# Kernel tuning notes

Measured on AMD Instinct MI355X. Metric: run time of the kernel, lower is better.

The kernel has to match this reference:

```python
import jax, jax.numpy as jnp
import numpy as np

VOCAB = 50257
D_MODEL = 1024
RANK = 64
V1, V2 = 225, 224   # ceil(sqrt(vocab)), ceil(vocab/v1)
D1, D2 = 32, 32     # ceil(sqrt(d_model)), ceil(d_model/d1)
B, L = 4, 4096


def setup_inputs() -> dict:
    key = jax.random.key(0)
    ks = jax.random.split(key, 4)
    input_ids = jax.random.randint(ks[0], (B, L), 0, VOCAB, dtype=jnp.int32)
    core1_q = jax.random.randint(ks[1], (V1, 1, RANK, D1), -128, 128, dtype=jnp.int32).astype(jnp.int8)
    core2_q = jax.random.randint(ks[2], (V2, RANK, 1, D2), -128, 128, dtype=jnp.int32).astype(jnp.int8)
    phase_shift = jax.random.normal(ks[3], (RANK,), dtype=jnp.float32) * 0.02
    return {
        "input_ids": input_ids,
        "core1_q": core1_q,
        "core1_scale": jnp.float32(0.01),
        "core1_zp": jnp.float32(0.0),
        "core2_q": core2_q,
        "core2_scale": jnp.float32(0.01),
        "core2_zp": jnp.float32(0.0),
        "phase_shift": phase_shift,
    }


def reference(input_ids, core1_q, core1_scale, core1_zp, core2_q, core2_scale, core2_zp, phase_shift):
    # token index -> (row in core1, row in core2)
    idx1 = jnp.clip(input_ids // V2, 0, V1 - 1)  # [B, L]
    idx2 = jnp.clip(input_ids % V2, 0, V2 - 1)   # [B, L]

    # gather int8 rows first, then dequantize: (q - zp) * scale (same math as
    # dequantizing full cores then gathering, but avoids touching unused rows)
    c1 = (core1_q[idx1, 0].astype(jnp.float32) - core1_zp) * core1_scale     # [B, L, R, D1]
    c2 = (core2_q[idx2, :, 0].astype(jnp.float32) - core2_zp) * core2_scale  # [B, L, R, D2]

    # phase modulation on core1 along the rank axis
    c1 = c1 * jnp.cos(phase_shift)[None, None, :, None]

    # per-token rank contraction: [B,L,D1,D2] -> [B,L,D1*D2] -> slice d_model
    out = jnp.einsum('blrd,blrf->bldf', c1, c2).reshape(B, L, D1 * D2)
    return out[:, :, :D_MODEL]
```

## Files before the change

### kernel.cpp

```cpp
#include <hip/hip_runtime.h>
#include <hip/hip_bf16.h>
#include <math.h>

#define V1N   225
#define V2N   224
#define RANK  64
#define DDIM  32
#define ROWE  (RANK*DDIM)
#define TPW   2

typedef __bf16  bf16x8 __attribute__((ext_vector_type(8)));
typedef float  f32x16 __attribute__((ext_vector_type(16)));
typedef float  f32x4  __attribute__((ext_vector_type(4)));
typedef int    i32x4  __attribute__((ext_vector_type(4)));

__global__ __launch_bounds__(256) void prep_tables(
    const int* __restrict__ c1q, const int* __restrict__ c2q,
    const float* __restrict__ s1p, const float* __restrict__ z1p,
    const float* __restrict__ s2p, const float* __restrict__ z2p,
    const float* __restrict__ phase,
    __bf16* __restrict__ t1, __bf16* __restrict__ t2)
{
    __shared__ float cosv[RANK];
    __shared__ float lds[4][64 * 33];

    int t = threadIdx.x;
    if (t < RANK) cosv[t] = cosf(phase[t]);
    __syncthreads();

    int w    = t >> 6;
    int lane = t & 63;
    int v    = blockIdx.x * 4 + w;
    if (v >= V1N + V2N) return;

    bool is1 = (v < V1N);
    const int* src; __bf16* dst; float sc, zp;
    if (is1) { src = c1q + (size_t)v * ROWE;            dst = t1 + (size_t)v * ROWE;  sc = *s1p; zp = *z1p; }
    else     { int u = v - V1N; src = c2q + (size_t)u * ROWE; dst = t2 + (size_t)u * ROWE; sc = *s2p; zp = *z2p; }

    float* L = lds[w];
    #pragma unroll
    for (int p = 0; p < 4; ++p) {
        i32x4 q0 = reinterpret_cast<const i32x4*>(src)[p * 128 + lane * 2];
        i32x4 q1 = reinterpret_cast<const i32x4*>(src)[p * 128 + lane * 2 + 1];
        #pragma unroll
        for (int j = 0; j < 8; ++j) {
            int e = p * 512 + lane * 8 + j;
            int q = (j < 4) ? q0[j & 3] : q1[j & 3];
            float val = ((float)q - zp) * sc;
            if (is1) val *= cosv[e >> 5];
            L[(e >> 5) * 33 + (e & 31)] = val;
        }
    }
    #pragma unroll
    for (int h = 0; h < 4; ++h) {
        int d   = lane >> 1;
        int rr0 = (lane & 1) * 8;
        bf16x8 o8;
        #pragma unroll
        for (int j = 0; j < 8; ++j) {
            int r = h * 16 + rr0 + j;
            o8[j] = (__bf16)L[r * 33 + d];
        }
        *reinterpret_cast<bf16x8*>(dst + h * 512 + lane * 8) = o8;
    }
}

__global__ __launch_bounds__(256) void tt_main(
    const int* __restrict__ ids,
    const __bf16* __restrict__ t1, const __bf16* __restrict__ t2,
    float* __restrict__ out, int n_tok)
{
    __shared__ float tile[4][32 * 36];

    int w    = threadIdx.x >> 6;
    int lane = threadIdx.x & 63;
    int m = lane & 31;
    int g = lane >> 5;
    int t0 = (blockIdx.x * 4 + w) * TPW;
    if (t0 >= n_tok) return;

    int aoff[TPW], boff[TPW];
    #pragma unroll
    for (int i = 0; i < TPW; ++i) {
        int t = t0 + i; if (t > n_tok - 1) t = n_tok - 1;
        unsigned id = (unsigned)ids[t];
        unsigned i1 = id / 224u; if (i1 > (unsigned)(V1N - 1)) i1 = V1N - 1;
        unsigned i2 = id % 224u;
        aoff[i] = (int)(i2 * ROWE);
        boff[i] = (int)(i1 * ROWE);
    }
    const __bf16* abase = t2 + m * 16 + g * 8;
    const __bf16* bbase = t1 + m * 16 + g * 8;

    bf16x8 aC[4], bC[4];
    #pragma unroll
    for (int s = 0; s < 4; ++s) {
        aC[s] = *reinterpret_cast<const bf16x8*>(abase + aoff[0] + s * 512);
        bC[s] = *reinterpret_cast<const bf16x8*>(bbase + boff[0] + s * 512);
    }

    float* tp = tile[w];
    #pragma unroll
    for (int k = 0; k < TPW; ++k) {
        bf16x8 aN[4], bN[4];
        if (k + 1 < TPW) {
            #pragma unroll
            for (int s = 0; s < 4; ++s) {
                aN[s] = *reinterpret_cast<const bf16x8*>(abase + aoff[k + 1] + s * 512);
                bN[s] = *reinterpret_cast<const bf16x8*>(bbase + boff[k + 1] + s * 512);
            }
        }

        f32x16 acc;
        #pragma unroll
        for (int i = 0; i < 16; ++i) acc[i] = 0.0f;
        #pragma unroll
        for (int s = 0; s < 4; ++s)
            acc = __builtin_amdgcn_mfma_f32_32x32x16_bf16(aC[s], bC[s], acc, 0, 0, 0);

        #pragma unroll
        for (int q = 0; q < 4; ++q) {
            f32x4 v = { acc[4 * q + 0], acc[4 * q + 1], acc[4 * q + 2], acc[4 * q + 3] };
            *reinterpret_cast<f32x4*>(tp + m * 36 + 8 * q + 4 * g) = v;
        }

        int tok = t0 + k;
        if (tok < n_tok) {
            float* o = out + (size_t)tok * 1024;
            #pragma unroll
            for (int p = 0; p < 4; ++p) {
                int d1 = p * 8 + (lane >> 3);
                int d2 = (lane & 7) * 4;
                f32x4 v = *reinterpret_cast<const f32x4*>(tp + d1 * 36 + d2);
                __builtin_nontemporal_store(v, reinterpret_cast<f32x4*>(o + p * 256 + lane * 4));
            }
        }

        if (k + 1 < TPW) {
            #pragma unroll
            for (int s = 0; s < 4; ++s) { aC[s] = aN[s]; bC[s] = bN[s]; }
        }
    }
}

__global__ __launch_bounds__(256) void tt_fused(
    const int* __restrict__ ids,
    const int* __restrict__ c1q, const int* __restrict__ c2q,
    const float* __restrict__ s1p, const float* __restrict__ z1p,
    const float* __restrict__ s2p, const float* __restrict__ z2p,
    const float* __restrict__ phase,
    float* __restrict__ out, int n_tok)
{
    __shared__ float cosv[RANK];
    if (threadIdx.x < RANK) cosv[threadIdx.x] = cosf(phase[threadIdx.x]);
    __syncthreads();

    int wave = (blockIdx.x << 2) + (threadIdx.x >> 6);
    if (wave >= n_tok) return;
    int lane = threadIdx.x & 63;
    int m = lane & 31;
    int g = lane >> 5;

    float s1 = *s1p, z1 = *z1p, s2 = *s2p, z2 = *z2p;

    unsigned id = (unsigned)ids[wave];
    unsigned i1 = id / 224u; if (i1 > (unsigned)(V1N - 1)) i1 = V1N - 1;
    unsigned i2 = id % 224u;

    const int* a_src = c2q + (size_t)i2 * ROWE + m;
    const int* b_src = c1q + (size_t)i1 * ROWE + m;

    f32x16 acc;
    #pragma unroll
    for (int i = 0; i < 16; ++i) acc[i] = 0.0f;

    #pragma unroll
    for (int s = 0; s < 4; ++s) {
        bf16x8 a, b;
        #pragma unroll
        for (int j = 0; j < 8; ++j) {
            int r = s * 16 + g * 8 + j;
            a[j] = (__bf16)((((float)a_src[r * 32]) - z2) * s2);
            b[j] = (__bf16)((((float)b_src[r * 32]) - z1) * s1 * cosv[r]);
        }
        acc = __builtin_amdgcn_mfma_f32_32x32x16_bf16(a, b, acc, 0, 0, 0);
    }

    float* o = out + (size_t)wave * 1024 + m * 32 + g * 4;
    #pragma unroll
    for (int q = 0; q < 4; ++q) {
        f32x4 v = { acc[4 * q + 0], acc[4 * q + 1], acc[4 * q + 2], acc[4 * q + 3] };
        __builtin_nontemporal_store(v, reinterpret_cast<f32x4*>(o + 8 * q));
    }
}

extern "C" void kernel_launch(void* const* d_in, const int* in_sizes, int n_in,
                              void* d_out, int out_size, void* d_ws, size_t ws_size,
                              hipStream_t stream) {
    const int*   ids = (const int*)d_in[0];
    const int*   c1q = (const int*)d_in[1];
    const float* s1  = (const float*)d_in[2];
    const float* z1  = (const float*)d_in[3];
    const int*   c2q = (const int*)d_in[4];
    const float* s2  = (const float*)d_in[5];
    const float* z2  = (const float*)d_in[6];
    const float* ph  = (const float*)d_in[7];
    float* out = (float*)d_out;

    int n_tok = in_sizes[0];
    int grid  = (n_tok + 4 * TPW - 1) / (4 * TPW);

    size_t need = (size_t)(V1N + V2N) * ROWE * sizeof(__bf16);
    if (ws_size >= need) {
        __bf16* t1 = (__bf16*)d_ws;
        __bf16* t2 = t1 + (size_t)V1N * ROWE;
        prep_tables<<<(V1N + V2N + 3) / 4, 256, 0, stream>>>(c1q, c2q, s1, z1, s2, z2, ph, t1, t2);
        tt_main<<<grid, 256, 0, stream>>>(ids, t1, t2, out, n_tok);
    } else {
        int fgrid = (n_tok + 3) / 4;
        tt_fused<<<fgrid, 256, 0, stream>>>(ids, c1q, c2q, s1, z1, s2, z2, ph, out, n_tok);
    }
}
```

Baseline: 23.52 us.

## Split waves into MFMA producers and store consumers with double-buffered LDS tiles

Restructures the main kernel so two waves per block gather table rows and run the MFMA contraction while the other two waves read the previous result tile from LDS and stream it to global memory. Tiles are double-buffered in shared memory and the block synchronises once per iteration, with each block handling eight tokens instead of eight spread over four independent waves. The aim is to overlap the output write traffic with compute. In exchange, half the waves do no math, the block-wide barriers add stalls, and the register prefetch of the next token's rows is gone.

```diff
diff --git a/kernel.cpp b/kernel.cpp
--- a/kernel.cpp
+++ b/kernel.cpp
@@ -5,9 +5,9 @@
 #define V1N   225
 #define V2N   224
 #define RANK  64
-#define DDIM  32
-#define ROWE  (RANK*DDIM)
-#define TPW   2
+#define ROWE  (RANK*32)
+#define PW    2
+#define NITER 4
 
 typedef __bf16  bf16x8 __attribute__((ext_vector_type(8)));
 typedef float  f32x16 __attribute__((ext_vector_type(16)));
@@ -66,81 +66,73 @@
     }
 }
 
-__global__ __launch_bounds__(256) void tt_main(
+__global__ __launch_bounds__(256, 8) void tt_main(
     const int* __restrict__ ids,
     const __bf16* __restrict__ t1, const __bf16* __restrict__ t2,
     float* __restrict__ out, int n_tok)
 {
-    __shared__ float tile[4][32 * 36];
+    __shared__ float tile[PW][2][32 * 36];
 
     int w    = threadIdx.x >> 6;
     int lane = threadIdx.x & 63;
     int m = lane & 31;
     int g = lane >> 5;
-    int t0 = (blockIdx.x * 4 + w) * TPW;
-    if (t0 >= n_tok) return;
-
-    int aoff[TPW], boff[TPW];
-    #pragma unroll
-    for (int i = 0; i < TPW; ++i) {
-        int t = t0 + i; if (t > n_tok - 1) t = n_tok - 1;
-        unsigned id = (unsigned)ids[t];
-        unsigned i1 = id / 224u; if (i1 > (unsigned)(V1N - 1)) i1 = V1N - 1;
-        unsigned i2 = id % 224u;
-        aoff[i] = (int)(i2 * ROWE);
-        boff[i] = (int)(i1 * ROWE);
+    bool producer = (w < PW);
+    int pw = w & (PW - 1);
+    int blk0 = blockIdx.x * (PW * NITER);
+
+    int aoff[NITER], boff[NITER];
+    if (producer) {
+        #pragma unroll
+        for (int r = 0; r < NITER; ++r) {
+            int t = blk0 + r * PW + pw; if (t > n_tok - 1) t = n_tok - 1;
+            unsigned id = (unsigned)ids[t];
+            unsigned i1 = id / 224u; if (i1 > (unsigned)(V1N - 1)) i1 = V1N - 1;
+            unsigned i2 = id % 224u;
+            aoff[r] = (int)(i2 * ROWE);
+            boff[r] = (int)(i1 * ROWE);
+        }
     }
     const __bf16* abase = t2 + m * 16 + g * 8;
     const __bf16* bbase = t1 + m * 16 + g * 8;
 
-    bf16x8 aC[4], bC[4];
-    #pragma unroll
-    for (int s = 0; s < 4; ++s) {
-        aC[s] = *reinterpret_cast<const bf16x8*>(abase + aoff[0] + s * 512);
-        bC[s] = *reinterpret_cast<const bf16x8*>(bbase + boff[0] + s * 512);
-    }
-
-    float* tp = tile[w];
-    #pragma unroll
-    for (int k = 0; k < TPW; ++k) {
-        bf16x8 aN[4], bN[4];
-        if (k + 1 < TPW) {
-            #pragma unroll
-            for (int s = 0; s < 4; ++s) {
-                aN[s] = *reinterpret_cast<const bf16x8*>(abase + aoff[k + 1] + s * 512);
-                bN[s] = *reinterpret_cast<const bf16x8*>(bbase + boff[k + 1] + s * 512);
+    #pragma unroll
+    for (int r = 0; r <= NITER; ++r) {
+        if (producer) {
+            if (r < NITER) {
+                f32x16 acc;
+                #pragma unroll
+                for (int i = 0; i < 16; ++i) acc[i] = 0.0f;
+                #pragma unroll
+                for (int s = 0; s < 4; ++s) {
+                    bf16x8 a = *reinterpret_cast<const bf16x8*>(abase + aoff[r] + s * 512);
+                    bf16x8 b = *reinterpret_cast<const bf16x8*>(bbase + boff[r] + s * 512);
+                    acc = __builtin_amdgcn_mfma_f32_32x32x16_bf16(a, b, acc, 0, 0, 0);
+                }
+                float* tp = tile[pw][r & 1];
+                #pragma unroll
+                for (int q = 0; q < 4; ++q) {
+                    f32x4 v = { acc[4 * q + 0], acc[4 * q + 1], acc[4 * q + 2], acc[4 * q + 3] };
+                    *reinterpret_cast<f32x4*>(tp + m * 36 + 8 * q + 4 * g) = v;
+                }
             }
-        }
-
-        f32x16 acc;
-        #pragma unroll
-        for (int i = 0; i < 16; ++i) acc[i] = 0.0f;
-        #pragma unroll
-        for (int s = 0; s < 4; ++s)
-            acc = __builtin_amdgcn_mfma_f32_32x32x16_bf16(aC[s], bC[s], acc, 0, 0, 0);
-
-        #pragma unroll
-        for (int q = 0; q < 4; ++q) {
-            f32x4 v = { acc[4 * q + 0], acc[4 * q + 1], acc[4 * q + 2], acc[4 * q + 3] };
-            *reinterpret_cast<f32x4*>(tp + m * 36 + 8 * q + 4 * g) = v;
-        }
-
-        int tok = t0 + k;
-        if (tok < n_tok) {
-            float* o = out + (size_t)tok * 1024;
-            #pragma unroll
-            for (int p = 0; p < 4; ++p) {
-                int d1 = p * 8 + (lane >> 3);
-                int d2 = (lane & 7) * 4;
-                f32x4 v = *reinterpret_cast<const f32x4*>(tp + d1 * 36 + d2);
-                __builtin_nontemporal_store(v, reinterpret_cast<f32x4*>(o + p * 256 + lane * 4));
+        } else {
+            if (r >= 1) {
+                int tok = blk0 + (r - 1) * PW + pw;
+                const float* tp = tile[pw][(r - 1) & 1];
+                if (tok < n_tok) {
+                    float* o = out + (size_t)tok * 1024;
+                    #pragma unroll
+                    for (int p = 0; p < 4; ++p) {
+                        int d1 = p * 8 + (lane >> 3);
+                        int d2 = (lane & 7) * 4;
+                        f32x4 v = *reinterpret_cast<const f32x4*>(tp + d1 * 36 + d2);
+                        __builtin_nontemporal_store(v, reinterpret_cast<f32x4*>(o + p * 256 + lane * 4));
+                    }
+                }
             }
         }
-
-        if (k + 1 < TPW) {
-            #pragma unroll
-            for (int s = 0; s < 4; ++s) { aC[s] = aN[s]; bC[s] = bN[s]; }
-        }
+        __syncthreads();
     }
 }
 
@@ -209,7 +201,8 @@
     float* out = (float*)d_out;
 
     int n_tok = in_sizes[0];
-    int grid  = (n_tok + 4 * TPW - 1) / (4 * TPW);
+    int tpb   = PW * NITER;
+    int grid  = (n_tok + tpb - 1) / tpb;
 
     size_t need = (size_t)(V1N + V2N) * ROWE * sizeof(__bf16);
     if (ws_size >= need) {
```

New measurement: 24.14 us. +2.6%, slower.
